# Optimization experiments

Measured on AMD Instinct MI355X. Metric: run time of the kernel, lower is better.

The kernel has to match this reference:

```python
import jax, jax.numpy as jnp
import numpy as np

B, L, HID = 2, 2048, 512
NUM_HEADS = 8
HEAD_DIM = HID // NUM_HEADS
GAP_ROWS = 33   # num_time_gap_buckets + 1
DUR_ROWS = 17   # num_duration_buckets + 1
NEG = -1e9      # finite stand-in for -inf (grad-safe, masked probs ~0)


def setup_inputs() -> dict:
    key = jax.random.key(0)
    ks = jax.random.split(key, 16)
    s = 1.0 / np.sqrt(HID)
    x = jax.random.normal(ks[0], (B, L, HID), dtype=jnp.float32)
    attention_mask = jax.random.randint(ks[1], (B, L), 0, 2, dtype=jnp.int32)
    time_gap_bucket_ids = jax.random.randint(ks[2], (B, L), 0, GAP_ROWS, dtype=jnp.int32)
    duration_bucket_ids = jax.random.randint(ks[3], (B, L), 0, DUR_ROWS, dtype=jnp.int32)
    Wq = jax.random.normal(ks[4], (HID, HID), dtype=jnp.float32) * s
    bq = jnp.zeros((HID,), jnp.float32)
    Wk = jax.random.normal(ks[5], (HID, HID), dtype=jnp.float32) * s
    bk = jnp.zeros((HID,), jnp.float32)
    Wv = jax.random.normal(ks[6], (HID, HID), dtype=jnp.float32) * s
    bv = jnp.zeros((HID,), jnp.float32)
    Wo = jax.random.normal(ks[7], (HID, HID), dtype=jnp.float32) * s
    bo = jnp.zeros((HID,), jnp.float32)
    # bias tables: padding_idx=0 row kept at zero, rest random for a meaningful test
    gap_emb = jax.random.normal(ks[8], (GAP_ROWS, NUM_HEADS), dtype=jnp.float32) * 0.1
    gap_emb = gap_emb.at[0].set(0.0)
    dur_emb = jax.random.normal(ks[9], (DUR_ROWS, NUM_HEADS), dtype=jnp.float32) * 0.1
    dur_emb = dur_emb.at[0].set(0.0)
    return dict(x=x, attention_mask=attention_mask,
                time_gap_bucket_ids=time_gap_bucket_ids,
                duration_bucket_ids=duration_bucket_ids,
                Wq=Wq, bq=bq, Wk=Wk, bk=bk, Wv=Wv, bv=bv, Wo=Wo, bo=bo,
                gap_emb=gap_emb, dur_emb=dur_emb)


def reference(x, attention_mask, time_gap_bucket_ids, duration_bucket_ids,
              Wq, bq, Wk, bk, Wv, bv, Wo, bo, gap_emb, dur_emb):
    b, l, hid = x.shape
    h, d = NUM_HEADS, HEAD_DIM
    def split_heads(t):  # (B,L,HID) -> (B,h,L,d)
        return t.reshape(b, l, h, d).transpose(0, 2, 1, 3)
    Q = split_heads(x @ Wq + bq)
    K = split_heads(x @ Wk + bk)
    V = split_heads(x @ Wv + bv)
    scores = jnp.einsum('bhqd,bhkd->bhqk', Q, K) / jnp.sqrt(jnp.float32(d))
    # relative time-gap bias: (B,L,L) bucket lookup -> (B,h,L,L)
    rel = jnp.abs(time_gap_bucket_ids[:, :, None] - time_gap_bucket_ids[:, None, :])
    rel = jnp.clip(rel, 0, GAP_ROWS - 1)
    gap_bias = gap_emb[rel]                       # (B,L,L,h)
    scores = scores + gap_bias.transpose(0, 3, 1, 2)
    # per-key duration bias: (B,L,h) -> (B,h,1,L)
    dur_bias = dur_emb[duration_bucket_ids]       # (B,L,h)
    scores = scores + dur_bias.transpose(0, 2, 1)[:, :, None, :]
    pad = (attention_mask == 0)[:, None, None, :]  # (B,1,1,L) over keys
    scores = jnp.where(pad, NEG, scores)
    attn = jax.nn.softmax(scores, axis=-1)
    out = jnp.einsum('bhqk,bhkd->bhqd', attn, V)
    out = out.transpose(0, 2, 1, 3).reshape(b, l, hid)
    return out @ Wo + bo
```

## Files before the change

### kernel.cpp

```cpp
#include <hip/hip_runtime.h>
#include <cmath>

typedef unsigned short u16;
typedef unsigned int   u32;
typedef __attribute__((ext_vector_type(2))) unsigned uintx2;
typedef __attribute__((ext_vector_type(4))) float    floatx4;
typedef __attribute__((ext_vector_type(4))) unsigned uintx4;
typedef __attribute__((ext_vector_type(8))) __bf16   bf16x8;

#define MFMA16(a, b, c) __builtin_amdgcn_mfma_f32_16x16x32_bf16((a), (b), (c), 0, 0, 0)

__device__ __forceinline__ u16 f2bf(float f) {
    union { float f; u32 u; } v; v.f = f;
    u32 u = v.u;
    return (u16)((u + 0x7FFFu + ((u >> 16) & 1u)) >> 16);
}

__device__ __forceinline__ bf16x8 ld_frag(const u16* p) {
    uintx4 t = *(const uintx4*)p;
    return __builtin_bit_cast(bf16x8, t);
}

#if __has_builtin(__builtin_amdgcn_exp2f)
#define EXP2F(x) __builtin_amdgcn_exp2f(x)
#else
#define EXP2F(x) exp2f(x)
#endif

typedef __attribute__((address_space(3))) unsigned       lds_u32;
typedef __attribute__((address_space(1))) const unsigned glb_u32;
__device__ __forceinline__ void gl_lds16(const void* g, void* l) {
    __builtin_amdgcn_global_load_lds((glb_u32*)(uintptr_t)g, (lds_u32*)(uintptr_t)l, 16, 0, 0);
}

#define LOG2E   1.4426950408889634f
#define QSCALE  0.18033688011112043f

__global__ __launch_bounds__(256) void prep_kernel(
        const float* __restrict__ x, const int* __restrict__ gap_ids,
        const int* __restrict__ dur_ids, const int* __restrict__ amask,
        const float* __restrict__ gap_emb, const float* __restrict__ dur_emb,
        u16* __restrict__ Xb, u16* __restrict__ Qe, u16* __restrict__ Ke) {
    int bid = blockIdx.x, tid = threadIdx.x;
    if (bid < 1024) {
        int idx = bid * 256 + tid;
        const float* src = x + (size_t)idx * 8;
        uintx4 o;
        o.x = f2bf(src[0]) | ((u32)f2bf(src[1]) << 16);
        o.y = f2bf(src[2]) | ((u32)f2bf(src[3]) << 16);
        o.z = f2bf(src[4]) | ((u32)f2bf(src[5]) << 16);
        o.w = f2bf(src[6]) | ((u32)f2bf(src[7]) << 16);
        *(uintx4*)(Xb + (size_t)idx * 8) = o;
    } else if (bid < 2048) {
        int ri = (bid - 1024) * 32 + (tid >> 3);
        int l = ri & 2047;
        int b = ri >> 14;
        int ch = tid & 7;
        int gq = gap_ids[b * 2048 + l];
        u16 lg = f2bf(LOG2E);
        u16 vals[8];
        for (int e = 0; e < 8; e++) {
            int j = ch * 8 + e;
            vals[e] = (j == gq || j == 33) ? lg : (u16)0;
        }
        *(uintx4*)(Qe + (size_t)ri * 128 + (8 + ch) * 8) = *(uintx4*)vals;
    } else {
        int ri = (bid - 2048) * 32 + (tid >> 3);
        int bh = ri >> 11, l = ri & 2047;
        int b = bh >> 3, h = bh & 7;
        int ch = tid & 7;
        int gk = gap_ids[b * 2048 + l];
        int did = dur_ids[b * 2048 + l];
        int msk = amask[b * 2048 + l];
        float kval = msk ? dur_emb[did * 8 + h] : -1e9f;
        u16 vals[8];
        for (int e = 0; e < 8; e++) {
            int j = ch * 8 + e;
            float v;
            if (j <= 32) { int d = j - gk; d = d < 0 ? -d : d; v = gap_emb[d * 8 + h]; }
            else if (j == 33) v = kval;
            else v = 0.f;
            vals[e] = f2bf(v);
        }
        int phys = 8 | (ch ^ (l & 7));
        *(uintx4*)(Ke + (size_t)ri * 128 + phys * 8) = *(uintx4*)vals;
    }
}

__global__ __launch_bounds__(256) void transpose_w_kernel(
        const float* __restrict__ Wq, const float* __restrict__ Wk,
        const float* __restrict__ Wv, const float* __restrict__ Wo,
        u16* __restrict__ WqT, u16* __restrict__ WkT,
        u16* __restrict__ WvT, u16* __restrict__ WoT) {
    __shared__ u16 T[64][72];
    int bid = blockIdx.x, tid = threadIdx.x;
    int mat = bid >> 6, t8 = bid & 63;
    int n0 = (t8 & 7) * 64, k0 = (t8 >> 3) * 64;
    const float* W = (mat == 0) ? Wq : (mat == 1) ? Wk : (mat == 2) ? Wv : Wo;
    u16* WT = (mat == 0) ? WqT : (mat == 1) ? WkT : (mat == 2) ? WvT : WoT;
    int r = tid >> 4, cq = tid & 15;
    for (int rr = 0; rr < 4; rr++) {
        int row = r + rr * 16;
        floatx4 s = *(const floatx4*)&W[(size_t)(k0 + row) * 512 + n0 + cq * 4];
        T[cq * 4 + 0][row] = f2bf(s.x);
        T[cq * 4 + 1][row] = f2bf(s.y);
        T[cq * 4 + 2][row] = f2bf(s.z);
        T[cq * 4 + 3][row] = f2bf(s.w);
    }
    __syncthreads();
    for (int p = 0; p < 2; p++) {
        int idx = p * 256 + tid;
        int c = idx >> 3, ch = idx & 7;
        *(uintx4*)&WT[(size_t)(n0 + c) * 512 + k0 + ch * 8] = *(const uintx4*)&T[c][ch * 8];
    }
}

__global__ __launch_bounds__(256) void gemm_qkv(
        const u16* __restrict__ Xb,
        const u16* __restrict__ WqT, const u16* __restrict__ WkT, const u16* __restrict__ WvT,
        const float* __restrict__ bq, const float* __restrict__ bk, const float* __restrict__ bv,
        u16* __restrict__ Qe, u16* __restrict__ Ke, u16* __restrict__ Vt) {
    __shared__ u16 smem[12288];
    u16* As = smem;
    u16* Bs = smem + 8192;

    int tid = threadIdx.x;
    int m0 = blockIdx.x * 128;
    int gy = blockIdx.y;
    int mat = gy >> 3, hh = gy & 7;
    int ncol0 = hh * 64;
    const u16* Bt = (mat == 0) ? WqT : (mat == 1) ? WkT : WvT;
    const float* bias = (mat == 0) ? bq : (mat == 1) ? bk : bv;

    int lane = tid & 63, w = tid >> 6, lo = lane & 15, hi = lane >> 4;
    int wm = w >> 1, wn = w & 1;
    floatx4 acc[4][2] = {};

    for (int kb = 0; kb < 8; kb++) {
        int k0 = kb * 64;
        __syncthreads();
        for (int it = 0; it < 4; it++) {
            int c = it * 256 + tid;
            int row = c >> 3, ch = c & 7;
            gl_lds16((const char*)Xb + ((size_t)(m0 + row) * 512 + k0) * 2 + ch * 16,
                     (char*)As + c * 16);
        }
        for (int it = 0; it < 2; it++) {
            int c = it * 256 + tid;
            int row = c >> 3, ch = c & 7;
            gl_lds16((const char*)Bt + ((size_t)(ncol0 + row) * 512 + k0) * 2 + ch * 16,
                     (char*)Bs + c * 16);
        }
        __syncthreads();
        for (int s = 0; s < 2; s++) {
            bf16x8 a[4], b[2];
            for (int i = 0; i < 4; i++)
                a[i] = ld_frag(&As[(64 * wm + 16 * i + lo) * 64 + s * 32 + hi * 8]);
            for (int j = 0; j < 2; j++)
                b[j] = ld_frag(&Bs[(32 * wn + 16 * j + lo) * 64 + s * 32 + hi * 8]);
            for (int i = 0; i < 4; i++)
                for (int j = 0; j < 2; j++)
                    acc[i][j] = MFMA16(a[i], b[j], acc[i][j]);
        }
    }

    int bb = m0 >> 11, l0 = m0 & 2047;
    __syncthreads();

    if (mat < 2) {
        u16* Ot = smem;
        for (int j = 0; j < 2; j++) {
            int col = 32 * wn + 16 * j + lo;
            float bval = bias[ncol0 + col];
            for (int i = 0; i < 4; i++) {
                int row = 64 * wm + 16 * i + 4 * hi;
                for (int r = 0; r < 4; r++) {
                    float v = acc[i][j][r] + bval;
                    if (mat == 0) v *= QSCALE;
                    Ot[(row + r) * 72 + col] = f2bf(v);
                }
            }
        }
        __syncthreads();
        for (int p = 0; p < 4; p++) {
            int cc = p * 256 + tid;
            int row = cc >> 3, ch = cc & 7;
            int lrow = l0 + row;
            size_t rowi = (size_t)(bb * 8 + hh) * 2048 + lrow;
            int ch2 = (mat == 1) ? (ch ^ (lrow & 7)) : ch;
            u16* dstp = (mat == 0) ? Qe : Ke;
            *(uintx4*)(dstp + rowi * 128 + ch2 * 8) = *(const uintx4*)(Ot + row * 72 + ch * 8);
        }
    } else {
        u16* Ot = smem;
        for (int j = 0; j < 2; j++) {
            int dc = 32 * wn + 16 * j + lo;
            float bval = bias[ncol0 + dc];
            for (int i = 0; i < 4; i++) {
                int row = 64 * wm + 16 * i + 4 * hi;
                for (int r = 0; r < 4; r++)
                    Ot[dc * 136 + row + r] = f2bf(acc[i][j][r] + bval);
            }
        }
        __syncthreads();
        for (int p = 0; p < 4; p++) {
            int cc = p * 256 + tid;
            int dc = cc >> 4, c16 = cc & 15;
            int grp = c16 >> 3, cp = c16 & 7;
            int s = dc & 15;
            int slot = cp ^ (s >> 1);
            uintx4 t = *(const uintx4*)(Ot + dc * 136 + c16 * 8);
            if (s & 1) { uintx4 u; u.x = t.z; u.y = t.w; u.z = t.x; u.w = t.y; t = u; }
            size_t dst = ((size_t)(bb * 8 + hh) * 64 + dc) * 2048 + l0 + grp * 64 + slot * 8;
            *(uintx4*)(Vt + dst) = t;
        }
    }
}

__global__ __launch_bounds__(256, 6) void flash_attn(
        const u16* __restrict__ Qe, const u16* __restrict__ Ke, const u16* __restrict__ Vt,
        float* __restrict__ Opart, float* __restrict__ Lpart) {
    __shared__ u16 Ks[64 * 128];
    __shared__ u16 Vs[64 * 64];

    int tid = threadIdx.x, lane = tid & 63, w = tid >> 6, lo = lane & 15, hi = lane >> 4;
    int qt = blockIdx.x, bh = blockIdx.y, sp = blockIdx.z;
    int q0 = qt * 64;
    int sw = lo & 7;

    size_t qrow = ((size_t)bh * 2048 + q0 + 16 * w + lo) * 128;
    bf16x8 bq_[4];
    for (int kc = 0; kc < 4; kc++) bq_[kc] = ld_frag(&Qe[qrow + kc * 32 + hi * 8]);

    floatx4 O[4] = {};
    floatx4 Lacc = {};
    uintx4 onesu; onesu.x = 0x3F803F80u; onesu.y = 0x3F803F80u; onesu.z = 0x3F803F80u; onesu.w = 0x3F803F80u;
    bf16x8 ones = __builtin_bit_cast(bf16x8, onesu);

    const u16* KeB = Ke + (size_t)bh * 2048 * 128;
    const u16* VtB = Vt + (size_t)bh * 64 * 2048;

    int kbeg = (sp * 32) / 3, kend = ((sp + 1) * 32) / 3;
    for (int kt = kbeg; kt < kend; kt++) {
        int k0 = kt * 64;
        __syncthreads();
        {
            const char* g = (const char*)(KeB + (size_t)k0 * 128);
            char* l = (char*)Ks;
            for (int r2 = 0; r2 < 4; r2++)
                gl_lds16(g + r2 * 4096 + tid * 16, l + r2 * 4096 + tid * 16);
        }
        {
            for (int p2 = 0; p2 < 2; p2++) {
                int c = p2 * 256 + tid;
                int row = c >> 3, ch = c & 7;
                const char* g = (const char*)(VtB + (size_t)row * 2048 + k0) + ch * 16;
                gl_lds16(g, (char*)Vs + c * 16);
            }
        }
        __syncthreads();

        floatx4 sf[4] = {};
        for (int t = 0; t < 4; t++) {
            const u16* krow = &Ks[(16 * t + lo) * 128];
            for (int kc = 0; kc < 4; kc++) {
                int cc = kc * 4 + hi;
                int pc = (cc & 8) | ((cc & 7) ^ sw);
                bf16x8 a = ld_frag(&krow[pc * 8]);
                sf[t] = MFMA16(a, bq_[kc], sf[t]);
            }
        }

        u32 pk[4][2];
        for (int t = 0; t < 4; t++) {
            float p0 = EXP2F(sf[t][0]);
            float p1 = EXP2F(sf[t][1]);
            float p2 = EXP2F(sf[t][2]);
            float p3 = EXP2F(sf[t][3]);
            u32 u0 = __builtin_bit_cast(u32, p0) + 0x8000u;
            u32 u1 = __builtin_bit_cast(u32, p1) + 0x8000u;
            u32 u2 = __builtin_bit_cast(u32, p2) + 0x8000u;
            u32 u3 = __builtin_bit_cast(u32, p3) + 0x8000u;
            pk[t][0] = __builtin_amdgcn_perm(u1, u0, 0x07060302);
            pk[t][1] = __builtin_amdgcn_perm(u3, u2, 0x07060302);
        }

        for (int tp = 0; tp < 2; tp++) {
            uintx4 av;
            av.x = pk[2 * tp][0]; av.y = pk[2 * tp][1];
            av.z = pk[2 * tp + 1][0]; av.w = pk[2 * tp + 1][1];
            bf16x8 af = __builtin_bit_cast(bf16x8, av);
            Lacc = MFMA16(af, ones, Lacc);
            for (int u = 0; u < 4; u++) {
                const u16* vrow = &Vs[(16 * u + lo) * 64];
                int c0 = (8 * tp + hi) ^ lo;
                int c1 = (8 * tp + 4 + hi) ^ lo;
                uintx2 lo64 = *(const uintx2*)&vrow[c0 * 4];
                uintx2 hi64 = *(const uintx2*)&vrow[c1 * 4];
                uintx4 bv;
                bv.x = lo64.x; bv.y = lo64.y; bv.z = hi64.x; bv.w = hi64.y;
                O[u] = MFMA16(af, __builtin_bit_cast(bf16x8, bv), O[u]);
            }
        }
    }

    size_t obase = (((size_t)sp * 16 + bh) * 32 + qt) * 4096;
    for (int u = 0; u < 4; u++)
        for (int r = 0; r < 4; r++)
            Opart[obase + (size_t)(16 * w + 4 * hi + r) * 64 + 16 * u + lo] = O[u][r];
    if (lo == 0) {
        size_t lbase = (((size_t)sp * 16 + bh) * 32 + qt) * 64;
        for (int r = 0; r < 4; r++) Lpart[lbase + 16 * w + 4 * hi + r] = Lacc[r];
    }
}

__global__ __launch_bounds__(256) void combine_kernel(const float* __restrict__ Opart,
                                                      const float* __restrict__ Lpart,
                                                      u16* __restrict__ Ob) {
    int idx = blockIdx.x * 256 + threadIdx.x;
    int d4 = idx & 15;
    int q = (idx >> 4) & 2047;
    int bh = idx >> 15;
    int qt = q >> 6, qr = q & 63;
    size_t b0 = ((size_t)bh * 32 + qt) * 4096 + qr * 64 + d4 * 4;
    floatx4 o0 = *(const floatx4*)&Opart[b0];
    floatx4 o1 = *(const floatx4*)&Opart[b0 + 2097152];
    floatx4 o2 = *(const floatx4*)&Opart[b0 + 4194304];
    size_t lb = ((size_t)bh * 32 + qt) * 64 + qr;
    float rl = 1.0f / (Lpart[lb] + Lpart[lb + 32768] + Lpart[lb + 65536]);
    uintx2 pk2;
    pk2.x = f2bf((o0.x + o1.x + o2.x) * rl) | ((u32)f2bf((o0.y + o1.y + o2.y) * rl) << 16);
    pk2.y = f2bf((o0.z + o1.z + o2.z) * rl) | ((u32)f2bf((o0.w + o1.w + o2.w) * rl) << 16);
    int bb = bh >> 3, h = bh & 7;
    *(uintx2*)&Ob[((size_t)(bb * 2048 + q)) * 512 + h * 64 + d4 * 4] = pk2;
}

__global__ __launch_bounds__(256) void gemm_out(
        const u16* __restrict__ Ob, const u16* __restrict__ WoT,
        const float* __restrict__ bo, float* __restrict__ out) {
    __shared__ u16 As[64][72];
    __shared__ u16 Bs[64][72];
    int tid = threadIdx.x;
    int m0 = blockIdx.x * 64;
    int n0 = blockIdx.y * 64;
    int lane = tid & 63, w = tid >> 6, lo = lane & 15, hi = lane >> 4;
    floatx4 acc[4] = {};

    for (int kb = 0; kb < 8; kb++) {
        __syncthreads();
        for (int c = tid; c < 512; c += 256) {
            int row = c >> 3, cc = c & 7;
            *(uintx4*)&As[row][cc * 8] =
                *(const uintx4*)&Ob[(size_t)(m0 + row) * 512 + kb * 64 + cc * 8];
            *(uintx4*)&Bs[row][cc * 8] =
                *(const uintx4*)&WoT[(size_t)(n0 + row) * 512 + kb * 64 + cc * 8];
        }
        __syncthreads();
        for (int s = 0; s < 2; s++) {
            bf16x8 a = ld_frag(&As[16 * w + lo][8 * hi + 32 * s]);
            for (int t = 0; t < 4; t++) {
                bf16x8 b = ld_frag(&Bs[16 * t + lo][8 * hi + 32 * s]);
                acc[t] = MFMA16(a, b, acc[t]);
            }
        }
    }
    for (int t = 0; t < 4; t++) {
        int n = n0 + 16 * t + lo;
        float bval = bo[n];
        for (int r = 0; r < 4; r++) {
            int mrow = m0 + 16 * w + 4 * hi + r;
            out[(size_t)mrow * 512 + n] = acc[t][r] + bval;
        }
    }
}

extern "C" void kernel_launch(void* const* d_in, const int* in_sizes, int n_in,
                              void* d_out, int out_size, void* d_ws, size_t ws_size,
                              hipStream_t stream) {
    const float* x     = (const float*)d_in[0];
    const int*   amask = (const int*)d_in[1];
    const int*   gids  = (const int*)d_in[2];
    const int*   dids  = (const int*)d_in[3];
    const float* Wq    = (const float*)d_in[4];
    const float* bq    = (const float*)d_in[5];
    const float* Wk    = (const float*)d_in[6];
    const float* bk    = (const float*)d_in[7];
    const float* Wv    = (const float*)d_in[8];
    const float* bv    = (const float*)d_in[9];
    const float* Wo    = (const float*)d_in[10];
    const float* bo    = (const float*)d_in[11];
    const float* gap_emb = (const float*)d_in[12];
    const float* dur_emb = (const float*)d_in[13];
    float* out = (float*)d_out;

    char* ws = (char*)d_ws;
    u16*   Qe    = (u16*)(ws + 0);
    u16*   Ke    = (u16*)(ws + 8388608);
    u16*   Vt    = (u16*)(ws + 16777216);
    float* Opart = (float*)(ws + 20971520);
    float* Lpart = (float*)(ws + 46137344);
    u16*   Ob    = (u16*)(ws + 46530560);
    u16*   WoT   = (u16*)(ws + 50724864);
    u16*   Xb    = (u16*)(ws + 20971520);
    u16*   WqT   = (u16*)(ws + 25165824);
    u16*   WkT   = (u16*)(ws + 25690112);
    u16*   WvT   = (u16*)(ws + 26214400);

    hipLaunchKernelGGL(prep_kernel, dim3(3072), dim3(256), 0, stream,
                       x, gids, dids, amask, gap_emb, dur_emb, Xb, Qe, Ke);
    hipLaunchKernelGGL(transpose_w_kernel, dim3(256), dim3(256), 0, stream,
                       Wq, Wk, Wv, Wo, WqT, WkT, WvT, WoT);
    hipLaunchKernelGGL(gemm_qkv, dim3(32, 24), dim3(256), 0, stream,
                       Xb, WqT, WkT, WvT, bq, bk, bv, Qe, Ke, Vt);
    hipLaunchKernelGGL(flash_attn, dim3(32, 16, 3), dim3(256), 0, stream,
                       Qe, Ke, Vt, Opart, Lpart);
    hipLaunchKernelGGL(combine_kernel, dim3(2048), dim3(256), 0, stream,
                       Opart, Lpart, Ob);
    hipLaunchKernelGGL(gemm_out, dim3(64, 8), dim3(256), 0, stream,
                       Ob, WoT, bo, out);
}
```

Measured before the change: 157.0 us.

## Process two query tiles per attention block with double-buffered K/V staging

Each flash-attention block now handles 128 queries (two 64-row groups), so every staged K/V tile feeds twice as many MFMAs and global K/V traffic per query is halved. The LDS loads are double-buffered: the next tile is issued before the current one is computed, which removes one barrier per iteration and overlaps load latency with compute. The V-transpose writer in the QKV GEMM is changed to a new swizzle so each PV B-fragment is read with one 16-byte LDS load instead of two 8-byte loads. In exchange, register and LDS use per block roughly double, the occupancy hint drops from 6 to 3, and the grid has half as many blocks (768).

```diff
diff --git a/kernel.cpp b/kernel.cpp
--- a/kernel.cpp
+++ b/kernel.cpp
@@ -204,36 +204,39 @@
         }
         __syncthreads();
         for (int p = 0; p < 4; p++) {
-            int cc = p * 256 + tid;
-            int dc = cc >> 4, c16 = cc & 15;
-            int grp = c16 >> 3, cp = c16 & 7;
-            int s = dc & 15;
-            int slot = cp ^ (s >> 1);
-            uintx4 t = *(const uintx4*)(Ot + dc * 136 + c16 * 8);
-            if (s & 1) { uintx4 u; u.x = t.z; u.y = t.w; u.z = t.x; u.w = t.y; t = u; }
-            size_t dst = ((size_t)(bb * 8 + hh) * 64 + dc) * 2048 + l0 + grp * 64 + slot * 8;
+            int cc4 = p * 256 + tid;
+            int dc = cc4 >> 4, c16 = cc4 & 15;
+            int g64 = c16 >> 3, phys = c16 & 7;
+            int mlog = phys ^ (dc & 7);
+            int g = mlog >> 2, q = mlog & 3;
+            int base = g64 * 64 + 32 * g + 4 * q;
+            uintx2 lo4 = *(const uintx2*)(Ot + dc * 136 + base);
+            uintx2 hi4 = *(const uintx2*)(Ot + dc * 136 + base + 16);
+            uintx4 t; t.x = lo4.x; t.y = lo4.y; t.z = hi4.x; t.w = hi4.y;
+            size_t dst = ((size_t)(bb * 8 + hh) * 64 + dc) * 2048 + l0 + g64 * 64 + phys * 8;
             *(uintx4*)(Vt + dst) = t;
         }
     }
 }
 
-__global__ __launch_bounds__(256, 6) void flash_attn(
+__global__ __launch_bounds__(256, 3) void flash_attn(
         const u16* __restrict__ Qe, const u16* __restrict__ Ke, const u16* __restrict__ Vt,
         float* __restrict__ Opart, float* __restrict__ Lpart) {
-    __shared__ u16 Ks[64 * 128];
-    __shared__ u16 Vs[64 * 64];
+    __shared__ u16 Ks[2][64 * 128];
+    __shared__ u16 Vs[2][64 * 64];
 
     int tid = threadIdx.x, lane = tid & 63, w = tid >> 6, lo = lane & 15, hi = lane >> 4;
-    int qt = blockIdx.x, bh = blockIdx.y, sp = blockIdx.z;
-    int q0 = qt * 64;
+    int qt2 = blockIdx.x, bh = blockIdx.y, sp = blockIdx.z;
     int sw = lo & 7;
 
-    size_t qrow = ((size_t)bh * 2048 + q0 + 16 * w + lo) * 128;
-    bf16x8 bq_[4];
-    for (int kc = 0; kc < 4; kc++) bq_[kc] = ld_frag(&Qe[qrow + kc * 32 + hi * 8]);
-
-    floatx4 O[4] = {};
-    floatx4 Lacc = {};
+    bf16x8 bq_[2][4];
+    for (int g = 0; g < 2; g++) {
+        size_t qrow = ((size_t)bh * 2048 + qt2 * 128 + g * 64 + 16 * w + lo) * 128;
+        for (int kc = 0; kc < 4; kc++) bq_[g][kc] = ld_frag(&Qe[qrow + kc * 32 + hi * 8]);
+    }
+
+    floatx4 O[2][4] = {};
+    floatx4 Lacc[2] = {};
     uintx4 onesu; onesu.x = 0x3F803F80u; onesu.y = 0x3F803F80u; onesu.z = 0x3F803F80u; onesu.w = 0x3F803F80u;
     bf16x8 ones = __builtin_bit_cast(bf16x8, onesu);
 
@@ -241,76 +244,90 @@
     const u16* VtB = Vt + (size_t)bh * 64 * 2048;
 
     int kbeg = (sp * 32) / 3, kend = ((sp + 1) * 32) / 3;
+
+#define STAGE(KT, BUF) do {                                                        \
+        int k0_ = (KT) * 64;                                                       \
+        const char* gk_ = (const char*)(KeB + (size_t)k0_ * 128);                  \
+        char* lk_ = (char*)Ks[BUF];                                                \
+        for (int r2 = 0; r2 < 4; r2++)                                             \
+            gl_lds16(gk_ + r2 * 4096 + tid * 16, lk_ + r2 * 4096 + tid * 16);      \
+        for (int p2 = 0; p2 < 2; p2++) {                                           \
+            int c_ = p2 * 256 + tid;                                               \
+            int row_ = c_ >> 3, ch_ = c_ & 7;                                      \
+            gl_lds16((const char*)(VtB + (size_t)row_ * 2048 + k0_) + ch_ * 16,    \
+                     (char*)Vs[BUF] + c_ * 16);                                    \
+        }                                                                          \
+    } while (0)
+
+    int cur = 0;
+    STAGE(kbeg, 0);
     for (int kt = kbeg; kt < kend; kt++) {
-        int k0 = kt * 64;
-        __syncthreads();
-        {
-            const char* g = (const char*)(KeB + (size_t)k0 * 128);
-            char* l = (char*)Ks;
-            for (int r2 = 0; r2 < 4; r2++)
-                gl_lds16(g + r2 * 4096 + tid * 16, l + r2 * 4096 + tid * 16);
-        }
-        {
-            for (int p2 = 0; p2 < 2; p2++) {
-                int c = p2 * 256 + tid;
-                int row = c >> 3, ch = c & 7;
-                const char* g = (const char*)(VtB + (size_t)row * 2048 + k0) + ch * 16;
-                gl_lds16(g, (char*)Vs + c * 16);
-            }
-        }
-        __syncthreads();
-
-        floatx4 sf[4] = {};
+        __syncthreads();
+        if (kt + 1 < kend) STAGE(kt + 1, cur ^ 1);
+
+        const u16* Ksc = Ks[cur];
+        const u16* Vsc = Vs[cur];
+
+        floatx4 sf[2][4] = {};
         for (int t = 0; t < 4; t++) {
-            const u16* krow = &Ks[(16 * t + lo) * 128];
+            const u16* krow = &Ksc[(16 * t + lo) * 128];
             for (int kc = 0; kc < 4; kc++) {
                 int cc = kc * 4 + hi;
                 int pc = (cc & 8) | ((cc & 7) ^ sw);
                 bf16x8 a = ld_frag(&krow[pc * 8]);
-                sf[t] = MFMA16(a, bq_[kc], sf[t]);
-            }
-        }
-
-        u32 pk[4][2];
-        for (int t = 0; t < 4; t++) {
-            float p0 = EXP2F(sf[t][0]);
-            float p1 = EXP2F(sf[t][1]);
-            float p2 = EXP2F(sf[t][2]);
-            float p3 = EXP2F(sf[t][3]);
-            u32 u0 = __builtin_bit_cast(u32, p0) + 0x8000u;
-            u32 u1 = __builtin_bit_cast(u32, p1) + 0x8000u;
-            u32 u2 = __builtin_bit_cast(u32, p2) + 0x8000u;
-            u32 u3 = __builtin_bit_cast(u32, p3) + 0x8000u;
-            pk[t][0] = __builtin_amdgcn_perm(u1, u0, 0x07060302);
-            pk[t][1] = __builtin_amdgcn_perm(u3, u2, 0x07060302);
+                sf[0][t] = MFMA16(a, bq_[0][kc], sf[0][t]);
+                sf[1][t] = MFMA16(a, bq_[1][kc], sf[1][t]);
+            }
+        }
+
+        bf16x8 af[2][2];
+        for (int g = 0; g < 2; g++) {
+            u32 pk[4][2];
+            for (int t = 0; t < 4; t++) {
+                float p0 = EXP2F(sf[g][t][0]);
+                float p1 = EXP2F(sf[g][t][1]);
+                float p2 = EXP2F(sf[g][t][2]);
+                float p3 = EXP2F(sf[g][t][3]);
+                u32 u0 = __builtin_bit_cast(u32, p0) + 0x8000u;
+                u32 u1 = __builtin_bit_cast(u32, p1) + 0x8000u;
+                u32 u2 = __builtin_bit_cast(u32, p2) + 0x8000u;
+                u32 u3 = __builtin_bit_cast(u32, p3) + 0x8000u;
+                pk[t][0] = __builtin_amdgcn_perm(u1, u0, 0x07060302);
+                pk[t][1] = __builtin_amdgcn_perm(u3, u2, 0x07060302);
+            }
+            for (int tp = 0; tp < 2; tp++) {
+                uintx4 av;
+                av.x = pk[2 * tp][0]; av.y = pk[2 * tp][1];
+                av.z = pk[2 * tp + 1][0]; av.w = pk[2 * tp + 1][1];
+                af[g][tp] = __builtin_bit_cast(bf16x8, av);
+            }
         }
 
         for (int tp = 0; tp < 2; tp++) {
-            uintx4 av;
-            av.x = pk[2 * tp][0]; av.y = pk[2 * tp][1];
-            av.z = pk[2 * tp + 1][0]; av.w = pk[2 * tp + 1][1];
-            bf16x8 af = __builtin_bit_cast(bf16x8, av);
-            Lacc = MFMA16(af, ones, Lacc);
+            Lacc[0] = MFMA16(af[0][tp], ones, Lacc[0]);
+            Lacc[1] = MFMA16(af[1][tp], ones, Lacc[1]);
             for (int u = 0; u < 4; u++) {
-                const u16* vrow = &Vs[(16 * u + lo) * 64];
-                int c0 = (8 * tp + hi) ^ lo;
-                int c1 = (8 * tp + 4 + hi) ^ lo;
-                uintx2 lo64 = *(const uintx2*)&vrow[c0 * 4];
-                uintx2 hi64 = *(const uintx2*)&vrow[c1 * 4];
-                uintx4 bv;
-                bv.x = lo64.x; bv.y = lo64.y; bv.z = hi64.x; bv.w = hi64.y;
-                O[u] = MFMA16(af, __builtin_bit_cast(bf16x8, bv), O[u]);
-            }
-        }
-    }
-
-    size_t obase = (((size_t)sp * 16 + bh) * 32 + qt) * 4096;
-    for (int u = 0; u < 4; u++)
-        for (int r = 0; r < 4; r++)
-            Opart[obase + (size_t)(16 * w + 4 * hi + r) * 64 + 16 * u + lo] = O[u][r];
-    if (lo == 0) {
-        size_t lbase = (((size_t)sp * 16 + bh) * 32 + qt) * 64;
-        for (int r = 0; r < 4; r++) Lpart[lbase + 16 * w + 4 * hi + r] = Lacc[r];
+                const u16* vrow = &Vsc[(16 * u + lo) * 64];
+                int m = (4 * tp + hi) ^ sw;
+                bf16x8 bv = ld_frag(&vrow[m * 8]);
+                O[0][u] = MFMA16(af[0][tp], bv, O[0][u]);
+                O[1][u] = MFMA16(af[1][tp], bv, O[1][u]);
+            }
+        }
+        cur ^= 1;
+    }
+#undef STAGE
+
+    for (int g = 0; g < 2; g++) {
+        int qt = 2 * qt2 + g;
+        size_t obase = (((size_t)sp * 16 + bh) * 32 + qt) * 4096;
+        for (int u = 0; u < 4; u++)
+            for (int r = 0; r < 4; r++)
+                Opart[obase + (size_t)(16 * w + 4 * hi + r) * 64 + 16 * u + lo] = O[g][u][r];
+        if (lo == 0) {
+            size_t lbase = (((size_t)sp * 16 + bh) * 32 + qt) * 64;
+            for (int r = 0; r < 4; r++) Lpart[lbase + 16 * w + 4 * hi + r] = Lacc[g][r];
+        }
     }
 }
 
@@ -412,7 +429,7 @@
                        Wq, Wk, Wv, Wo, WqT, WkT, WvT, WoT);
     hipLaunchKernelGGL(gemm_qkv, dim3(32, 24), dim3(256), 0, stream,
                        Xb, WqT, WkT, WvT, bq, bk, bv, Qe, Ke, Vt);
-    hipLaunchKernelGGL(flash_attn, dim3(32, 16, 3), dim3(256), 0, stream,
+    hipLaunchKernelGGL(flash_attn, dim3(16, 16, 3), dim3(256), 0, stream,
                        Qe, Ke, Vt, Opart, Lpart);
     hipLaunchKernelGGL(combine_kernel, dim3(2048), dim3(256), 0, stream,
                        Opart, Lpart, Ob);
```

After: 148.7 us. 1.06x faster.
